# Kernel tuning notes

Measured on AMD Instinct MI355X. Metric: run time of the kernel, lower is better.

The kernel has to match this reference:

```python
import jax, jax.numpy as jnp
import numpy as np
import math

IN_C, OUT_C = 64, 128
OUT_C1 = int((OUT_C - IN_C) * 0.3 + IN_C)  # 83
OUT_C2 = int((OUT_C - IN_C) * 0.6 + IN_C)  # 102
OUT_C3 = OUT_C                              # 128
RESIDUE_RATIO = 0.5
R_RES = math.sqrt(RESIDUE_RATIO)
R_SC = math.sqrt(1.0 - RESIDUE_RATIO)
PRELU_INIT = 0.25
POST_MEAN = (1.0 - PRELU_INIT) / math.sqrt(2.0 * math.pi)
_POST_EX2 = (1.0 + PRELU_INIT ** 2) / 2.0
POST_STDV = math.sqrt(_POST_EX2 - POST_MEAN ** 2)


def _conv1x1_weight(key, out_c, in_c):
    # torch Conv1d custom init: normal_, then divide by per-out-channel L2 norm
    w = jax.random.normal(key, (out_c, in_c), dtype=jnp.float32)
    norm = jnp.sqrt(jnp.sum(w ** 2, axis=1, keepdims=True) + 1e-8)
    return w / norm


def cprelu(x, w):
    # x: [B, C, N], w: [C]
    y = jnp.where(x >= 0, x, x * w[None, :, None])
    return (y - POST_MEAN) / POST_STDV


def setup_inputs() -> dict:
    key = jax.random.key(0)
    ks = jax.random.split(key, 8)
    x = jax.random.normal(ks[0], (16, IN_C, 8192), dtype=jnp.float32)
    conn = jax.random.uniform(ks[1], (4096, 8192), dtype=jnp.float32)
    return {
        "x": x,
        "conn": conn,
        "w1": _conv1x1_weight(ks[2], OUT_C1, IN_C),
        "b1": jnp.zeros((OUT_C1,), jnp.float32),
        "p1": jnp.full((OUT_C1,), PRELU_INIT, jnp.float32),
        "w2": _conv1x1_weight(ks[3], OUT_C2, OUT_C1),
        "b2": jnp.zeros((OUT_C2,), jnp.float32),
        "p2": jnp.full((OUT_C2,), PRELU_INIT, jnp.float32),
        "wm": _conv1x1_weight(ks[4], OUT_C3, OUT_C2),
        "bm": jnp.zeros((OUT_C3,), jnp.float32),
        "p3": jnp.full((OUT_C3,), PRELU_INIT, jnp.float32),
        "ws": _conv1x1_weight(ks[5], OUT_C, IN_C),
        "bs": jnp.zeros((OUT_C,), jnp.float32),
    }


def _forward(x, conn, w1, b1, p1, w2, b2, p2, wm, bm, p3, ws, bs):
    # self-connection matrix: binary mask of per-row argmax entries (ties kept)
    sc = (conn - jnp.max(conn, axis=1, keepdims=True) >= 0).astype(jnp.float32)

    # residue branch: 1x1 conv -> CPReLU -> 1x1 conv -> CPReLU -> Meshconv -> CPReLU
    h = cprelu(jnp.einsum('bcn,oc->bon', x, w1) + b1[None, :, None], p1)
    h = cprelu(jnp.einsum('bcn,oc->bon', h, w2) + b2[None, :, None], p2)
    h = jnp.einsum('bcn,oc->bon', h, wm) + bm[None, :, None]      # [B, C3, Nin]
    h = jnp.einsum('oi,bci->bco', conn, h)                         # mesh pooling -> [B, C3, Nout]
    res = cprelu(h, p3)

    # shortcut branch: Meshconv with self_connection_matrix (1x1 conv + pooled gather)
    s = jnp.einsum('bcn,oc->bon', x, ws) + bs[None, :, None]       # [B, OUT_C, Nin]
    s = jnp.einsum('oi,bci->bco', sc, s)                           # [B, OUT_C, Nout]

    return s * R_SC + res * R_RES


def reference(x, conn, w1, b1, p1, w2, b2, p2, wm, bm, p3, ws, bs):
    return _forward(x, conn, w1, b1, p1, w2, b2, p2, wm, bm, p3, ws, bs)
```

## Files before the change

### kernel.cpp

```cpp
#include <hip/hip_runtime.h>
#include <hip/hip_bf16.h>
#include <stdint.h>

using bf16x8 = __attribute__((ext_vector_type(8))) __bf16;
using bf16x4 = __attribute__((ext_vector_type(4))) __bf16;
using f32x4  = __attribute__((ext_vector_type(4))) float;

typedef const uint32_t __attribute__((address_space(1)))* gas_ptr;
typedef uint32_t __attribute__((address_space(3)))* las_ptr;

__device__ __forceinline__ void load_lds16(const void* g, void* l) {
    __builtin_amdgcn_global_load_lds((gas_ptr)g, (las_ptr)l, 16, 0, 0);
}

#define PM  0.29920671030107454f
#define PIS 1.5046096f
#define RHALF 0.70710678118654752f

#define MFMA __builtin_amdgcn_mfma_f32_16x16x32_bf16

__global__ __launch_bounds__(256) void k_prep(const float* __restrict__ w1,
                                              const float* __restrict__ w2,
                                              const float* __restrict__ wm,
                                              const float* __restrict__ wsw,
                                              __bf16* __restrict__ W1p,
                                              __bf16* __restrict__ W2p,
                                              __bf16* __restrict__ WMp,
                                              __bf16* __restrict__ WSp)
{
    const int id = blockIdx.x * 256 + threadIdx.x;
    const int stride = gridDim.x * 256;
    for (int i = id; i < 96 * 64; i += stride) {
        int oc = i >> 6, ic = i & 63;
        W1p[i] = (__bf16)((oc < 83) ? w1[oc * 64 + ic] : 0.f);
    }
    for (int i = id; i < 112 * 96; i += stride) {
        int oc = i / 96, ic = i % 96;
        W2p[i] = (__bf16)((oc < 102 && ic < 83) ? w2[oc * 83 + ic] : 0.f);
    }
    for (int i = id; i < 128 * 128; i += stride) {
        int oc = i >> 7, ic = i & 127;
        WMp[i] = (__bf16)((ic < 102) ? wm[oc * 102 + ic] : 0.f);
    }
    for (int i = id; i < 128 * 64; i += stride) {
        WSp[i] = (__bf16)wsw[i];
    }
}

__global__ __launch_bounds__(256) void k_cc(
    const float* __restrict__ conn, __bf16* __restrict__ cb, size_t rowstride,
    int* __restrict__ cnt, int* __restrict__ idx,
    const float* __restrict__ x,
    const float* __restrict__ b1, const float* __restrict__ p1,
    const float* __restrict__ b2, const float* __restrict__ p2,
    const float* __restrict__ bm, const float* __restrict__ bs,
    const __bf16* __restrict__ W1p, const __bf16* __restrict__ W2p,
    const __bf16* __restrict__ WMp, const __bf16* __restrict__ WSp,
    __bf16* __restrict__ h3, __bf16* __restrict__ s_t)
{
    __shared__ __align__(16) char pool[38528];
    const int t = threadIdx.x;
    const int bx = blockIdx.x;
    const int r3 = bx % 3;
    const int g  = bx / 3;

    if (r3 < 2) {
        const int o = 2 * g + r3;
        float* wmax = (float*)pool;
        int*   scnt = (int*)(pool + 16);
        const float* row = conn + (size_t)o * 8192;
        float4 v[8];
        float m = -1e30f;
#pragma unroll
        for (int q = 0; q < 8; q++) {
            v[q] = *(const float4*)(row + (size_t)(q * 256 + t) * 4);
            m = fmaxf(m, fmaxf(fmaxf(v[q].x, v[q].y), fmaxf(v[q].z, v[q].w)));
        }
        __syncthreads();
        __bf16* drow = cb + (size_t)o * rowstride;
#pragma unroll
        for (int q = 0; q < 8; q++) {
            bf16x4 w;
            w[0] = (__bf16)v[q].x; w[1] = (__bf16)v[q].y;
            w[2] = (__bf16)v[q].z; w[3] = (__bf16)v[q].w;
            *(bf16x4*)(drow + (size_t)(q * 256 + t) * 4) = w;
        }
#pragma unroll
        for (int off = 32; off > 0; off >>= 1) m = fmaxf(m, __shfl_down(m, off, 64));
        if ((t & 63) == 0) wmax[t >> 6] = m;
        if (t == 0) *scnt = 0;
        __syncthreads();
        const float rmax = fmaxf(fmaxf(wmax[0], wmax[1]), fmaxf(wmax[2], wmax[3]));
#pragma unroll
        for (int q = 0; q < 8; q++) {
            float vv[4] = {v[q].x, v[q].y, v[q].z, v[q].w};
#pragma unroll
            for (int e = 0; e < 4; e++) {
                if (vv[e] >= rmax) {
                    int p = atomicAdd(scnt, 1);
                    if (p < 16) idx[o * 16 + p] = (q * 256 + t) * 4 + e;
                }
            }
        }
        __syncthreads();
        if (t == 0) cnt[o] = *scnt < 16 ? *scnt : 16;
        return;
    }

    const int b  = g >> 7;
    const int p0 = (g & 127) * 64;
    __bf16* buf0 = (__bf16*)pool;
    __bf16* un   = (__bf16*)(pool + 17408);
    float*  bl   = (float*)(pool + 35840);
    __bf16* H1t  = un;
    __bf16* OutT = un;
    float* b1l = bl;       float* p1l = bl + 96;
    float* b2l = bl + 192; float* p2l = bl + 304;
    float* bml = bl + 416; float* bsl = bl + 544;

    const int lane = t & 63, wid = t >> 6;

    for (int i = t; i < 96; i += 256)  { b1l[i] = (i < 83)  ? b1[i] : 0.f; p1l[i] = (i < 83)  ? p1[i] : 0.f; }
    for (int i = t; i < 112; i += 256) { b2l[i] = (i < 102) ? b2[i] : 0.f; p2l[i] = (i < 102) ? p2[i] : 0.f; }
    for (int i = t; i < 128; i += 256) { bml[i] = bm[i]; bsl[i] = bs[i]; }

    {
        const int pg = (t & 15) * 4;
        const int c0 = t >> 4;
#pragma unroll
        for (int it = 0; it < 4; it++) {
            int c = it * 16 + c0;
            float4 xv = *(const float4*)(x + ((size_t)b * 64 + c) * 8192 + p0 + pg);
            buf0[(pg + 0) * 72 + c] = (__bf16)xv.x;
            buf0[(pg + 1) * 72 + c] = (__bf16)xv.y;
            buf0[(pg + 2) * 72 + c] = (__bf16)xv.z;
            buf0[(pg + 3) * 72 + c] = (__bf16)xv.w;
        }
    }
    __syncthreads();

    const int quad4 = (lane >> 4) << 2;
    const int l15 = lane & 15;
    const int kg  = (lane >> 4) << 3;
    const int nt  = wid;
    const int pos = nt * 16 + l15;

    bf16x8 xb0, xb1;
    {
        const __bf16* bp = buf0 + pos * 72 + kg;
        xb0 = *(const bf16x8*)(bp);
        xb1 = *(const bf16x8*)(bp + 32);
    }

#pragma unroll
    for (int mt = 0; mt < 8; mt++) {
        const __bf16* wp = WSp + (mt * 16 + l15) * 64 + kg;
        f32x4 a = {0.f, 0.f, 0.f, 0.f};
        a = MFMA(*(const bf16x8*)(wp),      xb0, a, 0, 0, 0);
        a = MFMA(*(const bf16x8*)(wp + 32), xb1, a, 0, 0, 0);
        int ocb = mt * 16 + quad4;
        bf16x4 ov;
#pragma unroll
        for (int r = 0; r < 4; r++) ov[r] = (__bf16)(a[r] + bsl[ocb + r]);
        *(bf16x4*)(s_t + ((size_t)b * 8192 + p0 + pos) * 128 + ocb) = ov;
    }

#pragma unroll
    for (int mt = 0; mt < 6; mt++) {
        const __bf16* wp = W1p + (mt * 16 + l15) * 64 + kg;
        f32x4 a = {0.f, 0.f, 0.f, 0.f};
        a = MFMA(*(const bf16x8*)(wp),      xb0, a, 0, 0, 0);
        a = MFMA(*(const bf16x8*)(wp + 32), xb1, a, 0, 0, 0);
        int ocb = mt * 16 + quad4;
        bf16x4 ov;
#pragma unroll
        for (int r = 0; r < 4; r++) {
            float v = a[r] + b1l[ocb + r];
            v = (v >= 0.f) ? v : v * p1l[ocb + r];
            ov[r] = (__bf16)((v - PM) * PIS);
        }
        *(bf16x4*)(&H1t[pos * 104 + ocb]) = ov;
    }
    __syncthreads();

    {
        bf16x8 hb[3];
        const __bf16* bp = H1t + pos * 104 + kg;
#pragma unroll
        for (int ks = 0; ks < 3; ks++) hb[ks] = *(const bf16x8*)(bp + ks * 32);
#pragma unroll
        for (int mt = 0; mt < 7; mt++) {
            const __bf16* wp = W2p + (mt * 16 + l15) * 96 + kg;
            f32x4 a = {0.f, 0.f, 0.f, 0.f};
#pragma unroll
            for (int ks = 0; ks < 3; ks++)
                a = MFMA(*(const bf16x8*)(wp + ks * 32), hb[ks], a, 0, 0, 0);
            int ocb = mt * 16 + quad4;
            bf16x4 ov;
#pragma unroll
            for (int r = 0; r < 4; r++) {
                float v = a[r] + b2l[ocb + r];
                v = (v >= 0.f) ? v : v * p2l[ocb + r];
                ov[r] = (__bf16)((v - PM) * PIS);
            }
            *(bf16x4*)(&buf0[pos * 136 + ocb]) = ov;
        }
    }
    for (int i = t; i < 64 * 16; i += 256) {
        int pp = i >> 4, c = 112 + (i & 15);
        buf0[pp * 136 + c] = (__bf16)0.f;
    }
    __syncthreads();

    {
        bf16x8 h2b[4];
        const __bf16* bp = buf0 + pos * 136 + kg;
#pragma unroll
        for (int ks = 0; ks < 4; ks++) h2b[ks] = *(const bf16x8*)(bp + ks * 32);
#pragma unroll
        for (int mt = 0; mt < 8; mt++) {
            const __bf16* wp = WMp + (mt * 16 + l15) * 128 + kg;
            f32x4 a = {0.f, 0.f, 0.f, 0.f};
#pragma unroll
            for (int ks = 0; ks < 4; ks++)
                a = MFMA(*(const bf16x8*)(wp + ks * 32), h2b[ks], a, 0, 0, 0);
            int ocb = mt * 16 + quad4;
#pragma unroll
            for (int r = 0; r < 4; r++)
                OutT[(ocb + r) * 72 + pos] = (__bf16)(a[r] + bml[ocb + r]);
        }
    }
    __syncthreads();

#pragma unroll
    for (int it = 0; it < 4; it++) {
        int lin = it * 256 + t;
        int ch = lin >> 3, pc = lin & 7;
        bf16x8 v = *(const bf16x8*)(OutT + ch * 72 + pc * 8);
        *(bf16x8*)(h3 + ((size_t)b * 128 + ch) * 8192 + p0 + pc * 8) = v;
    }
}

__global__ __launch_bounds__(256, 2) void k_gemm(const __bf16* __restrict__ A,
                                                 const __bf16* __restrict__ B,
                                                 size_t bstride,
                                                 float* __restrict__ out,
                                                 const __bf16* __restrict__ s_t,
                                                 const int* __restrict__ idx,
                                                 const int* __restrict__ cnt,
                                                 const float* __restrict__ p3)
{
    __shared__ __align__(16) char pool[66560];
    __bf16* la = (__bf16*)pool;
    __bf16* lb = (__bf16*)(pool + 16384);
    float*  sp = (float*)pool;
    float* p3l = (float*)(pool + 66048);

    const int t = threadIdx.x;
    const int lane = t & 63;
    const int wid = t >> 6;
    const int tMi = blockIdx.y;
    const int tM = tMi * 128;
    const int tN = blockIdx.x * 128;
    const int wm2 = (wid & 1) * 64;
    const int wn2 = (wid >> 1) * 64;

    f32x4 acc[4][4];
    const f32x4 zero = {0.f, 0.f, 0.f, 0.f};
#pragma unroll
    for (int i = 0; i < 4; i++)
#pragma unroll
        for (int j = 0; j < 4; j++) acc[i][j] = zero;

    const int tr = t >> 3;
    const int sc = (t & 7) ^ (tr & 7);
    const __bf16* pA[4];
    const __bf16* pB[4];
#pragma unroll
    for (int i = 0; i < 4; i++) {
        pA[i] = A + (size_t)(tM + i * 32 + tr) * 8192 + sc * 8;
        pB[i] = B + (size_t)(tN + i * 32 + tr) * bstride + sc * 8;
    }

    const int l15 = lane & 15;
    const int q = lane >> 4;
    int aoff[4], boff[4];
#pragma unroll
    for (int i = 0; i < 4; i++) {
        int row = wm2 + i * 16 + l15;
        aoff[i] = row * 64 + ((q ^ (row & 7)) * 8);
    }
#pragma unroll
    for (int j = 0; j < 4; j++) {
        int row = wn2 + j * 16 + l15;
        boff[j] = row * 64 + ((q ^ (row & 7)) * 8);
    }

    for (int it = 0; it < 128; it++) {
#pragma unroll
        for (int i = 0; i < 4; i++) load_lds16(pA[i], la + (i * 256 + t) * 8);
#pragma unroll
        for (int i = 0; i < 4; i++) load_lds16(pB[i], lb + (i * 256 + t) * 8);
#pragma unroll
        for (int i = 0; i < 4; i++) { pA[i] += 64; pB[i] += 64; }
        __syncthreads();
#pragma unroll
        for (int ks = 0; ks < 2; ks++) {
            bf16x8 af[4], bfr[4];
#pragma unroll
            for (int i = 0; i < 4; i++) af[i]  = *(const bf16x8*)(la + (aoff[i] ^ (ks << 5)));
#pragma unroll
            for (int j = 0; j < 4; j++) bfr[j] = *(const bf16x8*)(lb + (boff[j] ^ (ks << 5)));
#pragma unroll
            for (int i = 0; i < 4; i++)
#pragma unroll
                for (int j = 0; j < 4; j++)
                    acc[i][j] = MFMA(af[i], bfr[j], acc[i][j], 0, 0, 0);
        }
        __syncthreads();
    }

    {
        const int l = t >> 1;
        const int part = t & 1;
        const int col = tN + l;
        const int n = cnt[col];
        const __bf16* base = s_t + ((size_t)tMi * 8192) * 128 + part * 64;
        float* spr = sp + l * 129 + part * 64;
        {
            const __bf16* row = base + (size_t)idx[col * 16] * 128;
#pragma unroll
            for (int j = 0; j < 8; j++) {
                bf16x8 v = *(const bf16x8*)(row + j * 8);
#pragma unroll
                for (int u = 0; u < 8; u++) spr[j * 8 + u] = (float)v[u];
            }
        }
        for (int k = 1; k < n; k++) {
            const __bf16* row = base + (size_t)idx[col * 16 + k] * 128;
#pragma unroll
            for (int j = 0; j < 8; j++) {
                bf16x8 v = *(const bf16x8*)(row + j * 8);
#pragma unroll
                for (int u = 0; u < 8; u++) spr[j * 8 + u] += (float)v[u];
            }
        }
        if (t < 128) p3l[t] = p3[t];
    }
    __syncthreads();

    const int quad4 = q * 4;
#pragma unroll
    for (int i = 0; i < 4; i++) {
        int gm = tM + wm2 + i * 16 + quad4;
#pragma unroll
        for (int j = 0; j < 4; j++) {
            int gn = tN + wn2 + j * 16 + l15;
            int colT = wn2 + j * 16 + l15;
#pragma unroll
            for (int r = 0; r < 4; r++) {
                int c = wm2 + i * 16 + quad4 + r;
                float v = acc[i][j][r];
                float pw = p3l[c];
                float y = (v >= 0.f) ? v : v * pw;
                y = (y - PM) * PIS;
                out[(size_t)(gm + r) * 4096 + gn] = sp[colT * 129 + c] * RHALF + y * RHALF;
            }
        }
    }
}

extern "C" void kernel_launch(void* const* d_in, const int* in_sizes, int n_in,
                              void* d_out, int out_size, void* d_ws, size_t ws_size,
                              hipStream_t stream) {
    (void)in_sizes; (void)n_in; (void)out_size;
    const float* x    = (const float*)d_in[0];
    const float* conn = (const float*)d_in[1];
    const float* w1   = (const float*)d_in[2];
    const float* b1   = (const float*)d_in[3];
    const float* p1   = (const float*)d_in[4];
    const float* w2   = (const float*)d_in[5];
    const float* b2   = (const float*)d_in[6];
    const float* p2   = (const float*)d_in[7];
    const float* wm   = (const float*)d_in[8];
    const float* bm   = (const float*)d_in[9];
    const float* p3   = (const float*)d_in[10];
    const float* wsw  = (const float*)d_in[11];
    const float* bs   = (const float*)d_in[12];
    float* out = (float*)d_out;

    char* ws = (char*)d_ws;
    __bf16* h3  = (__bf16*)(ws);
    __bf16* s_t = (__bf16*)(ws + 33554432);
    __bf16* W1p = (__bf16*)(ws + 67108864);
    __bf16* W2p = (__bf16*)(ws + 67108864 + 12288);
    __bf16* WMp = (__bf16*)(ws + 67108864 + 33792);
    __bf16* WSp = (__bf16*)(ws + 67108864 + 66560);
    int* idx = (int*)(ws + 67108864 + 82944);
    int* cnt = (int*)(ws + 67108864 + 82944 + 262144);
    const size_t connb_off = 67108864 + 82944 + 262144 + 16384;

    __bf16* connb;
    size_t  cstride;
    if (ws_size >= connb_off + (size_t)4096 * 8192 * 2) {
        connb = (__bf16*)(ws + connb_off);
        cstride = 8192;
    } else {
        connb = (__bf16*)const_cast<float*>(conn);
        cstride = 16384;
    }

    k_prep<<<32, 256, 0, stream>>>(w1, w2, wm, wsw, W1p, W2p, WMp, WSp);
    k_cc<<<6144, 256, 0, stream>>>(conn, connb, cstride, cnt, idx,
                                   x, b1, p1, b2, p2, bm, bs,
                                   W1p, W2p, WMp, WSp, h3, s_t);
    k_gemm<<<dim3(32, 16), 256, 0, stream>>>(h3, connb, cstride, out, s_t, idx, cnt, p3);
}
```

Before: 470.5 us.

## Split-K the mesh pooling GEMM and move epilogue into separate combine kernel

```diff
diff --git a/kernel.cpp b/kernel.cpp
--- a/kernel.cpp
+++ b/kernel.cpp
@@ -241,131 +241,153 @@
     }
 }
 
-__global__ __launch_bounds__(256, 2) void k_gemm(const __bf16* __restrict__ A,
+__global__ __launch_bounds__(256, 4) void k_gemm(const __bf16* __restrict__ A,
                                                  const __bf16* __restrict__ B,
                                                  size_t bstride,
-                                                 float* __restrict__ out,
+                                                 float* __restrict__ C0,
+                                                 float* __restrict__ C1,
+                                                 int KH)
+{
+    __shared__ __bf16 la[128 * 64];
+    __shared__ __bf16 lb[128 * 64];
+    const int t = threadIdx.x;
+    const int lane = t & 63;
+    const int wid = t >> 6;
+    const int tM = blockIdx.y * 128;
+    const int tN = blockIdx.x * 128;
+    const int kz = blockIdx.z;
+    const int k0 = kz * KH;
+    float* __restrict__ C = kz ? C1 : C0;
+    const int wm2 = (wid & 1) * 64;
+    const int wn2 = (wid >> 1) * 64;
+
+    f32x4 acc[4][4];
+    const f32x4 zero = {0.f, 0.f, 0.f, 0.f};
+#pragma unroll
+    for (int i = 0; i < 4; i++)
+#pragma unroll
+        for (int j = 0; j < 4; j++) acc[i][j] = zero;
+
+    const int tr = t >> 3;
+    const int sc = (t & 7) ^ (tr & 7);
+    const __bf16* pA[4];
+    const __bf16* pB[4];
+#pragma unroll
+    for (int i = 0; i < 4; i++) {
+        pA[i] = A + (size_t)(tM + i * 32 + tr) * 8192 + k0 + sc * 8;
+        pB[i] = B + (size_t)(tN + i * 32 + tr) * bstride + k0 + sc * 8;
+    }
+
+    const int l15 = lane & 15;
+    const int q = lane >> 4;
+    int aoff[4], boff[4];
+#pragma unroll
+    for (int i = 0; i < 4; i++) {
+        int row = wm2 + i * 16 + l15;
+        aoff[i] = row * 64 + ((q ^ (row & 7)) * 8);
+    }
+#pragma unroll
+    for (int j = 0; j < 4; j++) {
+        int row = wn2 + j * 16 + l15;
+        boff[j] = row * 64 + ((q ^ (row & 7)) * 8);
+    }
+
+    const int iters = KH >> 6;
+    for (int it = 0; it < iters; it++) {
+#pragma unroll
+        for (int i = 0; i < 4; i++) load_lds16(pA[i], la + (i * 256 + t) * 8);
+#pragma unroll
+        for (int i = 0; i < 4; i++) load_lds16(pB[i], lb + (i * 256 + t) * 8);
+#pragma unroll
+        for (int i = 0; i < 4; i++) { pA[i] += 64; pB[i] += 64; }
+        __syncthreads();
+#pragma unroll
+        for (int ks = 0; ks < 2; ks++) {
+            bf16x8 af[4], bfr[4];
+#pragma unroll
+            for (int i = 0; i < 4; i++) af[i]  = *(const bf16x8*)(la + (aoff[i] ^ (ks << 5)));
+#pragma unroll
+            for (int j = 0; j < 4; j++) bfr[j] = *(const bf16x8*)(lb + (boff[j] ^ (ks << 5)));
+#pragma unroll
+            for (int i = 0; i < 4; i++)
+#pragma unroll
+                for (int j = 0; j < 4; j++)
+                    acc[i][j] = MFMA(af[i], bfr[j], acc[i][j], 0, 0, 0);
+        }
+        __syncthreads();
+    }
+
+    const int quad4 = (lane >> 4) * 4;
+#pragma unroll
+    for (int i = 0; i < 4; i++) {
+        int gm = tM + wm2 + i * 16 + quad4;
+#pragma unroll
+        for (int j = 0; j < 4; j++) {
+            int gn = tN + wn2 + j * 16 + l15;
+#pragma unroll
+            for (int r = 0; r < 4; r++)
+                C[(size_t)(gm + r) * 4096 + gn] = acc[i][j][r];
+        }
+    }
+}
+
+__global__ __launch_bounds__(256) void k_combine(float* __restrict__ out,
+                                                 const float* __restrict__ P1,
+                                                 int nsplit,
                                                  const __bf16* __restrict__ s_t,
                                                  const int* __restrict__ idx,
                                                  const int* __restrict__ cnt,
                                                  const float* __restrict__ p3)
 {
-    __shared__ __align__(16) char pool[66560];
-    __bf16* la = (__bf16*)pool;
-    __bf16* lb = (__bf16*)(pool + 16384);
-    float*  sp = (float*)pool;
-    float* p3l = (float*)(pool + 66048);
-
+    __shared__ float sp[64][133];
+    const int b = blockIdx.y;
+    const int o0 = blockIdx.x * 64;
     const int t = threadIdx.x;
-    const int lane = t & 63;
-    const int wid = t >> 6;
-    const int tMi = blockIdx.y;
-    const int tM = tMi * 128;
-    const int tN = blockIdx.x * 128;
-    const int wm2 = (wid & 1) * 64;
-    const int wn2 = (wid >> 1) * 64;
-
-    f32x4 acc[4][4];
-    const f32x4 zero = {0.f, 0.f, 0.f, 0.f};
-#pragma unroll
-    for (int i = 0; i < 4; i++)
-#pragma unroll
-        for (int j = 0; j < 4; j++) acc[i][j] = zero;
-
-    const int tr = t >> 3;
-    const int sc = (t & 7) ^ (tr & 7);
-    const __bf16* pA[4];
-    const __bf16* pB[4];
-#pragma unroll
-    for (int i = 0; i < 4; i++) {
-        pA[i] = A + (size_t)(tM + i * 32 + tr) * 8192 + sc * 8;
-        pB[i] = B + (size_t)(tN + i * 32 + tr) * bstride + sc * 8;
-    }
-
-    const int l15 = lane & 15;
-    const int q = lane >> 4;
-    int aoff[4], boff[4];
-#pragma unroll
-    for (int i = 0; i < 4; i++) {
-        int row = wm2 + i * 16 + l15;
-        aoff[i] = row * 64 + ((q ^ (row & 7)) * 8);
-    }
-#pragma unroll
-    for (int j = 0; j < 4; j++) {
-        int row = wn2 + j * 16 + l15;
-        boff[j] = row * 64 + ((q ^ (row & 7)) * 8);
-    }
-
-    for (int it = 0; it < 128; it++) {
-#pragma unroll
-        for (int i = 0; i < 4; i++) load_lds16(pA[i], la + (i * 256 + t) * 8);
-#pragma unroll
-        for (int i = 0; i < 4; i++) load_lds16(pB[i], lb + (i * 256 + t) * 8);
-#pragma unroll
-        for (int i = 0; i < 4; i++) { pA[i] += 64; pB[i] += 64; }
-        __syncthreads();
-#pragma unroll
-        for (int ks = 0; ks < 2; ks++) {
-            bf16x8 af[4], bfr[4];
-#pragma unroll
-            for (int i = 0; i < 4; i++) af[i]  = *(const bf16x8*)(la + (aoff[i] ^ (ks << 5)));
-#pragma unroll
-            for (int j = 0; j < 4; j++) bfr[j] = *(const bf16x8*)(lb + (boff[j] ^ (ks << 5)));
-#pragma unroll
-            for (int i = 0; i < 4; i++)
-#pragma unroll
-                for (int j = 0; j < 4; j++)
-                    acc[i][j] = MFMA(af[i], bfr[j], acc[i][j], 0, 0, 0);
-        }
-        __syncthreads();
-    }
 
     {
-        const int l = t >> 1;
-        const int part = t & 1;
-        const int col = tN + l;
-        const int n = cnt[col];
-        const __bf16* base = s_t + ((size_t)tMi * 8192) * 128 + part * 64;
-        float* spr = sp + l * 129 + part * 64;
-        {
-            const __bf16* row = base + (size_t)idx[col * 16] * 128;
-#pragma unroll
-            for (int j = 0; j < 8; j++) {
-                bf16x8 v = *(const bf16x8*)(row + j * 8);
-#pragma unroll
-                for (int u = 0; u < 8; u++) spr[j * 8 + u] = (float)v[u];
+        const int ol = t >> 2;
+        const int part = t & 3;
+        const int o = o0 + ol;
+        const int n = cnt[o];
+        float acc[32];
+#pragma unroll
+        for (int j = 0; j < 32; j++) acc[j] = 0.f;
+        for (int k = 0; k < n; k++) {
+            const int i = idx[o * 16 + k];
+            const __bf16* row = s_t + ((size_t)b * 8192 + i) * 128 + part * 32;
+#pragma unroll
+            for (int j = 0; j < 32; j += 8) {
+                bf16x8 v = *(const bf16x8*)(row + j);
+#pragma unroll
+                for (int u = 0; u < 8; u++) acc[j + u] += (float)v[u];
             }
         }
-        for (int k = 1; k < n; k++) {
-            const __bf16* row = base + (size_t)idx[col * 16 + k] * 128;
-#pragma unroll
-            for (int j = 0; j < 8; j++) {
-                bf16x8 v = *(const bf16x8*)(row + j * 8);
-#pragma unroll
-                for (int u = 0; u < 8; u++) spr[j * 8 + u] += (float)v[u];
-            }
-        }
-        if (t < 128) p3l[t] = p3[t];
+#pragma unroll
+        for (int j = 0; j < 32; j++) sp[ol][part * 32 + j] = acc[j];
     }
     __syncthreads();
 
-    const int quad4 = q * 4;
-#pragma unroll
-    for (int i = 0; i < 4; i++) {
-        int gm = tM + wm2 + i * 16 + quad4;
-#pragma unroll
-        for (int j = 0; j < 4; j++) {
-            int gn = tN + wn2 + j * 16 + l15;
-            int colT = wn2 + j * 16 + l15;
-#pragma unroll
-            for (int r = 0; r < 4; r++) {
-                int c = wm2 + i * 16 + quad4 + r;
-                float v = acc[i][j][r];
-                float pw = p3l[c];
-                float y = (v >= 0.f) ? v : v * pw;
-                y = (y - PM) * PIS;
-                out[(size_t)(gm + r) * 4096 + gn] = sp[colT * 129 + c] * RHALF + y * RHALF;
-            }
+    if (nsplit == 2) {
+        for (int rr = 0; rr < 32; rr++) {
+            const int c = rr * 4 + (t >> 6);
+            const int o = t & 63;
+            const size_t oi = ((size_t)b * 128 + c) * 4096 + o0 + o;
+            float v = out[oi] + P1[oi];
+            const float pw = p3[c];
+            float y = (v >= 0.f) ? v : v * pw;
+            y = (y - PM) * PIS;
+            out[oi] = sp[o][c] * RHALF + y * RHALF;
+        }
+    } else {
+        for (int rr = 0; rr < 32; rr++) {
+            const int c = rr * 4 + (t >> 6);
+            const int o = t & 63;
+            const size_t oi = ((size_t)b * 128 + c) * 4096 + o0 + o;
+            float v = out[oi];
+            const float pw = p3[c];
+            float y = (v >= 0.f) ? v : v * pw;
+            y = (y - PM) * PIS;
+            out[oi] = sp[o][c] * RHALF + y * RHALF;
         }
     }
 }
@@ -398,7 +420,9 @@
     __bf16* WSp = (__bf16*)(ws + 67108864 + 66560);
     int* idx = (int*)(ws + 67108864 + 82944);
     int* cnt = (int*)(ws + 67108864 + 82944 + 262144);
-    const size_t connb_off = 67108864 + 82944 + 262144 + 16384;
+    const size_t p1_off    = 67108864 + 82944 + 262144 + 16384;
+    float* Pk1 = (float*)(ws + p1_off);
+    const size_t connb_off = p1_off + 33554432;
 
     __bf16* connb;
     size_t  cstride;
@@ -409,10 +433,14 @@
         connb = (__bf16*)const_cast<float*>(conn);
         cstride = 16384;
     }
+    const int nsplit = (ws_size >= p1_off + 33554432) ? 2 : 1;
+    const int KH = 8192 / nsplit;
 
     k_prep<<<32, 256, 0, stream>>>(w1, w2, wm, wsw, W1p, W2p, WMp, WSp);
     k_cc<<<6144, 256, 0, stream>>>(conn, connb, cstride, cnt, idx,
                                    x, b1, p1, b2, p2, bm, bs,
                                    W1p, W2p, WMp, WSp, h3, s_t);
-    k_gemm<<<dim3(32, 16), 256, 0, stream>>>(h3, connb, cstride, out, s_t, idx, cnt, p3);
-}
+    k_gemm<<<dim3(4096 / 128, 2048 / 128, nsplit), 256, 0, stream>>>(h3, connb, cstride,
+                                                                     out, Pk1, KH);
+    k_combine<<<dim3(4096 / 64, 16), 256, 0, stream>>>(out, Pk1, nsplit, s_t, idx, cnt, p3);
+}
```

Result: no change. 463.0 us (median of 2 runs) (-1.6%).
